# Performance work log

Hardware: AMD Instinct MI355X
Metric: run time of the kernel (lower is better)

The kernel has to match this reference:

```python
import jax, jax.numpy as jnp
import numpy as np

EPS = 1e-6
BETA = 0.25
COMMIT_W = 1.0


def setup_inputs() -> dict:
    key = jax.random.key(0)
    k1, k2, k3 = jax.random.split(key, 3)
    b, c, h, w = 8, 256, 32, 32
    n_e, e_dim = 16384, 256
    z = jax.random.normal(k1, (b, c, h, w), jnp.float32)
    # frozen_codebook = randn(n_e, e_dim) * e_dim**-0.5
    codebook = jax.random.normal(k2, (n_e, e_dim), jnp.float32) * (e_dim ** -0.5)
    # nn.Linear(e_dim, in_channels, bias=False) weight: (in_channels, e_dim)
    W = jax.random.normal(k3, (c, e_dim), jnp.float32) * (e_dim ** -0.5)
    return {"z": z, "codebook": codebook, "W": W}


def _rotate_to(src, tgt):
    # Rotation trick (Fifty et al.): rotate src onto tgt direction with a
    # detached Householder-style transform; gradient flows through src only.
    # src, tgt: (n, d)
    norm_src = jnp.linalg.norm(src, axis=-1, keepdims=True)
    norm_tgt = jnp.linalg.norm(tgt, axis=-1, keepdims=True)
    u = src / (norm_src + EPS)
    q = tgt / (norm_tgt + EPS)
    uq = u + q
    w_ = jax.lax.stop_gradient(uq / (jnp.linalg.norm(uq, axis=-1, keepdims=True) + EPS))
    u_d = jax.lax.stop_gradient(u)
    q_d = jax.lax.stop_gradient(q)
    rot = (src
           - 2.0 * jnp.sum(src * w_, axis=-1, keepdims=True) * w_
           + 2.0 * jnp.sum(src * u_d, axis=-1, keepdims=True) * q_d)
    return rot * jax.lax.stop_gradient(norm_tgt / (norm_src + EPS))


def reference(z, codebook, W):
    b, c, h, w = z.shape
    # b c h w -> (b*h*w, c)
    z_flat = jnp.transpose(z, (0, 2, 3, 1)).reshape(-1, c)
    # implicit codebook: frozen codes through linear projection
    emb = codebook @ W.T  # (n_e, c)
    # squared L2 distances (no grad needed for argmin)
    d = (jnp.sum(z_flat ** 2, axis=1, keepdims=True)
         + jnp.sum(emb ** 2, axis=1)
         - 2.0 * (z_flat @ emb.T))  # (n_tok, n_e)
    indices = jnp.argmin(d, axis=1)  # (n_tok,)
    z_q_flat = emb[indices]  # gather quantized vectors
    loss = COMMIT_W * (jnp.mean((jax.lax.stop_gradient(z_flat) - z_q_flat) ** 2)
                       + BETA * jnp.mean((z_flat - jax.lax.stop_gradient(z_q_flat)) ** 2))
    z_q_flat = _rotate_to(z_flat, z_q_flat)
    z_q = jnp.transpose(z_q_flat.reshape(b, h, w, c), (0, 3, 1, 2))
    return z_q, loss, indices
```

## Files before the change

### kernel.cpp

```cpp
#include <hip/hip_runtime.h>
#include <math.h>

#define EPSV 1e-6f
#define NTOK 8192
#define NE   16384
#define DIM  256

using short8 = __attribute__((ext_vector_type(8))) short;
using f32x4v = __attribute__((ext_vector_type(4))) float;

__device__ __forceinline__ unsigned short f2bf(float v) {
    unsigned int u = __float_as_uint(v);
    u += 0x7fffu + ((u >> 16) & 1u);
    return (unsigned short)(u >> 16);
}
__device__ __forceinline__ float bf2f(unsigned short h) {
    return __uint_as_float(((unsigned int)h) << 16);
}

__device__ __forceinline__ void gload_lds16(const void* g, void* s) {
    __builtin_amdgcn_global_load_lds(
        (const __attribute__((address_space(1))) void*)g,
        (__attribute__((address_space(3))) void*)s, 16, 0, 0);
}

__global__ __launch_bounds__(256) void k0a_transpose(
    const float* __restrict__ zin, float* __restrict__ z_flat,
    unsigned short* __restrict__ zh, unsigned short* __restrict__ zl) {
    __shared__ float tile[64][65];
    const int tid = threadIdx.x;
    const int yx0 = blockIdx.x * 64, c0 = blockIdx.y * 64, b = blockIdx.z;
    const int sub = tid >> 6, ln = tid & 63;
#pragma unroll
    for (int j = 0; j < 16; ++j) {
        int cl = j * 4 + sub;
        tile[cl][ln] = zin[((size_t)(b * 256 + c0 + cl) << 10) + yx0 + ln];
    }
    __syncthreads();
#pragma unroll
    for (int j = 0; j < 16; ++j) {
        int tl = j * 4 + sub;
        float v = tile[ln][tl];
        size_t o = (size_t)(b * 1024 + yx0 + tl) * 256 + c0 + ln;
        z_flat[o] = v;
        unsigned short h = f2bf(v);
        zh[o] = h;
        zl[o] = f2bf(v - bf2f(h));
    }
}

__global__ __launch_bounds__(256) void k0b_sz(const float* __restrict__ z_flat,
                                              float* __restrict__ sz) {
    const int w = threadIdx.x >> 6, lane = threadIdx.x & 63;
    const int t = blockIdx.x * 4 + w;
    const float4 v = *(const float4*)(z_flat + (size_t)t * 256 + lane * 4);
    double s = (double)v.x * v.x + (double)v.y * v.y + (double)v.z * v.z +
               (double)v.w * v.w;
#pragma unroll
    for (int m = 1; m < 64; m <<= 1) s += __shfl_xor(s, m);
    if (lane == 0) sz[t] = (float)s;
}

__global__ __launch_bounds__(256) void k0c_emb(
    const float* __restrict__ cb, const float* __restrict__ Wm,
    float* __restrict__ emb, unsigned short* __restrict__ eh,
    unsigned short* __restrict__ el) {
    __shared__ float cbS[64][68];
    __shared__ float wS[64][68];
    const int tid = threadIdx.x;
    const int n0 = blockIdx.x * 64, c0 = blockIdx.y * 64;
    const int tx = tid & 15, ty = tid >> 4;
    float acc[4][4] = {};
    for (int kc = 0; kc < 4; ++kc) {
        __syncthreads();
#pragma unroll
        for (int it = 0; it < 16; ++it) {
            int idx = it * 256 + tid;
            int rw = idx >> 6, kk = idx & 63;
            cbS[rw][kk] = cb[(size_t)(n0 + rw) * 256 + kc * 64 + kk];
            wS[rw][kk]  = Wm[(size_t)(c0 + rw) * 256 + kc * 64 + kk];
        }
        __syncthreads();
#pragma unroll
        for (int k4 = 0; k4 < 16; ++k4) {
            float4 ra[4], rb[4];
#pragma unroll
            for (int a = 0; a < 4; ++a)
                ra[a] = *(const float4*)&cbS[ty * 4 + a][k4 * 4];
#pragma unroll
            for (int bb = 0; bb < 4; ++bb)
                rb[bb] = *(const float4*)&wS[tx * 4 + bb][k4 * 4];
#pragma unroll
            for (int a = 0; a < 4; ++a)
#pragma unroll
                for (int bb = 0; bb < 4; ++bb)
                    acc[a][bb] += ra[a].x * rb[bb].x + ra[a].y * rb[bb].y +
                                  ra[a].z * rb[bb].z + ra[a].w * rb[bb].w;
        }
    }
#pragma unroll
    for (int a = 0; a < 4; ++a) {
        int n = n0 + ty * 4 + a;
#pragma unroll
        for (int bb = 0; bb < 4; ++bb) {
            int c = c0 + tx * 4 + bb;
            size_t o = (size_t)n * 256 + c;
            float v = acc[a][bb];
            emb[o] = v;
            unsigned short h = f2bf(v);
            eh[o] = h;
            el[o] = f2bf(v - bf2f(h));
        }
    }
}

__global__ __launch_bounds__(256) void k0d_se(const float* __restrict__ emb,
                                              float* __restrict__ se) {
    const int w = threadIdx.x >> 6, lane = threadIdx.x & 63;
    const int n = blockIdx.x * 4 + w;
    const float4 v = *(const float4*)(emb + (size_t)n * 256 + lane * 4);
    double s = (double)v.x * v.x + (double)v.y * v.y + (double)v.z * v.z +
               (double)v.w * v.w;
#pragma unroll
    for (int m = 1; m < 64; m <<= 1) s += __shfl_xor(s, m);
    if (lane == 0) se[n] = (float)s;
}

__global__ __launch_bounds__(256, 2) void k1_dist_argmin(
    const unsigned short* __restrict__ zh, const unsigned short* __restrict__ zl,
    const unsigned short* __restrict__ eh, const unsigned short* __restrict__ el,
    const float* __restrict__ sz, const float* __restrict__ se,
    float* __restrict__ pval, int* __restrict__ pidx) {
    __shared__ short8 smem[2][2048];
    const int tid = threadIdx.x;
    const int w = tid >> 6, lane = tid & 63;
    const int quad = lane >> 4, lr = lane & 15;
    const int tokBase = blockIdx.x * 128;
    const int rowBase = tokBase + w * 32;
    const int slab = blockIdx.y;
    const int slabBase = slab * 2048;

    short8 Ah[2][8], Al[2][8];
#pragma unroll
    for (int mt = 0; mt < 2; ++mt)
#pragma unroll
        for (int ks = 0; ks < 8; ++ks) {
            size_t o = (size_t)(rowBase + mt * 16 + lr) * 256 + ks * 32 + quad * 8;
            Ah[mt][ks] = *(const short8*)(zh + o);
            Al[mt][ks] = *(const short8*)(zl + o);
        }

    float szr[2][4];
#pragma unroll
    for (int mt = 0; mt < 2; ++mt)
#pragma unroll
        for (int rr = 0; rr < 4; ++rr)
            szr[mt][rr] = sz[rowBase + mt * 16 + quad * 4 + rr];

    float minv[2][4];
    int mini[2][4];
#pragma unroll
    for (int mt = 0; mt < 2; ++mt)
#pragma unroll
        for (int rr = 0; rr < 4; ++rr) {
            minv[mt][rr] = INFINITY;
            mini[mt][rr] = 0;
        }

    auto stage = [&](int buf, int ch) {
        const int colBase = slabBase + ch * 32;
#pragma unroll
        for (int i = 0; i < 8; ++i) {
            int u = i * 256 + tid;
            int fmt = u >> 10;
            int u1 = u & 1023;
            int col = u1 >> 5, kgs = u1 & 31;
            int kg = kgs ^ col;
            const unsigned short* g =
                (fmt ? el : eh) + (size_t)(colBase + col) * 256 + kg * 8;
            gload_lds16(g, (char*)&smem[buf][0] + (((size_t)i * 256 + w * 64) << 4));
        }
    };

    stage(0, 0);
    __syncthreads();

    for (int ch = 0; ch < 64; ++ch) {
        const int cur = ch & 1;
        if (ch + 1 < 64) stage(cur ^ 1, ch + 1);

        f32x4v acc[2][2];
#pragma unroll
        for (int mt = 0; mt < 2; ++mt)
#pragma unroll
            for (int nt = 0; nt < 2; ++nt)
                acc[mt][nt] = (f32x4v){0.f, 0.f, 0.f, 0.f};

#pragma unroll
        for (int ks = 0; ks < 8; ++ks) {
            short8 Bh[2], Bl[2];
#pragma unroll
            for (int nt = 0; nt < 2; ++nt) {
                int col = nt * 16 + lr;
                int kgs = (ks * 4 + quad) ^ col;
                Bh[nt] = smem[cur][col * 32 + kgs];
                Bl[nt] = smem[cur][1024 + col * 32 + kgs];
            }
#pragma unroll
            for (int mt = 0; mt < 2; ++mt)
#pragma unroll
                for (int nt = 0; nt < 2; ++nt) {
                    f32x4v a = acc[mt][nt];
                    a = __builtin_amdgcn_mfma_f32_16x16x32_bf16(Ah[mt][ks], Bh[nt], a, 0, 0, 0);
                    a = __builtin_amdgcn_mfma_f32_16x16x32_bf16(Ah[mt][ks], Bl[nt], a, 0, 0, 0);
                    a = __builtin_amdgcn_mfma_f32_16x16x32_bf16(Al[mt][ks], Bh[nt], a, 0, 0, 0);
                    acc[mt][nt] = a;
                }
        }

        const int colBase = slabBase + ch * 32;
#pragma unroll
        for (int nt = 0; nt < 2; ++nt) {
            const int colg = colBase + nt * 16 + lr;
            const float sec = se[colg];
#pragma unroll
            for (int mt = 0; mt < 2; ++mt)
#pragma unroll
                for (int rr = 0; rr < 4; ++rr) {
                    float d = __fsub_rn(__fadd_rn(szr[mt][rr], sec),
                                        2.0f * acc[mt][nt][rr]);
                    if (d < minv[mt][rr]) {
                        minv[mt][rr] = d;
                        mini[mt][rr] = colg;
                    }
                }
        }
        __syncthreads();
    }

#pragma unroll
    for (int st = 1; st < 16; st <<= 1) {
#pragma unroll
        for (int mt = 0; mt < 2; ++mt)
#pragma unroll
            for (int rr = 0; rr < 4; ++rr) {
                float ov = __shfl_xor(minv[mt][rr], st);
                int oi = __shfl_xor(mini[mt][rr], st);
                if (ov < minv[mt][rr] ||
                    (ov == minv[mt][rr] && oi < mini[mt][rr])) {
                    minv[mt][rr] = ov;
                    mini[mt][rr] = oi;
                }
            }
    }
    if (lr == 0) {
#pragma unroll
        for (int mt = 0; mt < 2; ++mt)
#pragma unroll
            for (int rr = 0; rr < 4; ++rr) {
                int row = rowBase + mt * 16 + quad * 4 + rr;
                pval[(size_t)row * 8 + slab] = minv[mt][rr];
                pidx[(size_t)row * 8 + slab] = mini[mt][rr];
            }
    }
}

__global__ __launch_bounds__(256) void k3a_token(
    const float* __restrict__ z_flat, const float* __restrict__ emb,
    const float* __restrict__ pval, const int* __restrict__ pidx,
    float* __restrict__ alpha, float* __restrict__ beta,
    int* __restrict__ idxf, float* __restrict__ out,
    float* __restrict__ lpart) {
    __shared__ float red[4];
    const int w = threadIdx.x >> 6, lane = threadIdx.x & 63;
    const int t = blockIdx.x * 4 + w;
    int best = 0;
    if (lane == 0) {
        float bv = INFINITY;
        int bi = 0;
#pragma unroll
        for (int s = 0; s < 8; ++s) {
            float v = pval[(size_t)t * 8 + s];
            int ii = pidx[(size_t)t * 8 + s];
            if (v < bv || (v == bv && ii < bi)) { bv = v; bi = ii; }
        }
        best = bi;
    }
    best = __shfl(best, 0);

    const float4 zv = *(const float4*)(z_flat + (size_t)t * 256 + lane * 4);
    const float4 ev = *(const float4*)(emb + (size_t)best * 256 + lane * 4);
    float szs = zv.x * zv.x + zv.y * zv.y + zv.z * zv.z + zv.w * zv.w;
    float ses = ev.x * ev.x + ev.y * ev.y + ev.z * ev.z + ev.w * ev.w;
    float zes = zv.x * ev.x + zv.y * ev.y + zv.z * ev.z + zv.w * ev.w;
    float dx = zv.x - ev.x, dy = zv.y - ev.y, dz = zv.z - ev.z, dw = zv.w - ev.w;
    float sqs = dx * dx + dy * dy + dz * dz + dw * dw;
#pragma unroll
    for (int m = 1; m < 64; m <<= 1) {
        szs += __shfl_xor(szs, m);
        ses += __shfl_xor(ses, m);
        zes += __shfl_xor(zes, m);
        sqs += __shfl_xor(sqs, m);
    }
    if (lane == 0) {
        float ns = sqrtf(szs), nt = sqrtf(ses);
        float inv_s = 1.0f / (ns + EPSV);
        float inv_t = 1.0f / (nt + EPSV);
        float s2 = szs * inv_s;
        float su = szs * inv_s * inv_s;
        float sq = ses * inv_t * inv_t;
        float uq = zes * inv_s * inv_t;
        float nw = sqrtf(su + sq + 2.0f * uq);
        float inv_w = 1.0f / (nw + EPSV);
        float s1 = (s2 + zes * inv_t) * inv_w;
        float scale = nt * inv_s;
        float a = scale * (1.0f - 2.0f * s1 * inv_w * inv_s);
        float bb = scale * inv_t * 2.0f * (s2 - s1 * inv_w);
        alpha[t] = a;
        beta[t] = bb;
        idxf[t] = best;
        out[2097153 + t] = (float)best;
        red[w] = sqs;
    }
    __syncthreads();
    if (threadIdx.x == 0)
        lpart[blockIdx.x] = red[0] + red[1] + red[2] + red[3];
}

__global__ __launch_bounds__(256) void k4_loss(float* __restrict__ out,
                                               const float* __restrict__ lpart) {
    __shared__ float red[4];
    const int tid = threadIdx.x;
    float s = 0.0f;
    for (int i = tid; i < 2048; i += 256) s += lpart[i];
#pragma unroll
    for (int m = 1; m < 64; m <<= 1) s += __shfl_xor(s, m);
    if ((tid & 63) == 0) red[tid >> 6] = s;
    __syncthreads();
    if (tid == 0)
        out[2097152] = 1.25f * (red[0] + red[1] + red[2] + red[3]) *
                       (1.0f / 2097152.0f);
}

__global__ __launch_bounds__(256) void k3b_zq(
    const float* __restrict__ zin, const float* __restrict__ emb,
    const float* __restrict__ alpha, const float* __restrict__ beta,
    const int* __restrict__ idxf, float* __restrict__ out) {
    const int i = blockIdx.x * 256 + threadIdx.x;
    const int c = (i >> 10) & 255;
    const int t = ((i >> 18) << 10) | (i & 1023);
    out[i] = alpha[t] * zin[i] + beta[t] * emb[(size_t)idxf[t] * 256 + c];
}

extern "C" void kernel_launch(void* const* d_in, const int* in_sizes, int n_in,
                              void* d_out, int out_size, void* d_ws,
                              size_t ws_size, hipStream_t stream) {
    (void)in_sizes; (void)n_in; (void)out_size; (void)ws_size;
    const float* zin = (const float*)d_in[0];
    const float* cb  = (const float*)d_in[1];
    const float* Wm  = (const float*)d_in[2];
    float* out = (float*)d_out;
    char* ws = (char*)d_ws;

    float*          z_flat = (float*)(ws + 0);
    unsigned short* zh     = (unsigned short*)(ws + 8388608);
    unsigned short* zl     = (unsigned short*)(ws + 12582912);
    float*          emb    = (float*)(ws + 16777216);
    unsigned short* eh     = (unsigned short*)(ws + 33554432);
    unsigned short* el     = (unsigned short*)(ws + 41943040);
    float*          sz     = (float*)(ws + 50331648);
    float*          se     = (float*)(ws + 50364416);
    float*          pval   = (float*)(ws + 50429952);
    int*            pidx   = (int*)(ws + 50692096);
    float*          alpha  = (float*)(ws + 50954240);
    float*          beta   = (float*)(ws + 50987008);
    int*            idxf   = (int*)(ws + 51019776);
    float*          lpart  = (float*)(ws + 51052544);

    k0a_transpose<<<dim3(16, 4, 8), 256, 0, stream>>>(zin, z_flat, zh, zl);
    k0b_sz<<<2048, 256, 0, stream>>>(z_flat, sz);
    k0c_emb<<<dim3(256, 4), 256, 0, stream>>>(cb, Wm, emb, eh, el);
    k0d_se<<<4096, 256, 0, stream>>>(emb, se);
    k1_dist_argmin<<<dim3(64, 8), 256, 0, stream>>>(zh, zl, eh, el, sz, se,
                                                    pval, pidx);
    k3a_token<<<2048, 256, 0, stream>>>(z_flat, emb, pval, pidx, alpha, beta,
                                        idxf, out, lpart);
    k4_loss<<<1, 256, 0, stream>>>(out, lpart);
    k3b_zq<<<8192, 256, 0, stream>>>(zin, emb, alpha, beta, idxf, out);
}
```

Baseline: 340.2 us.

## Use split-bf16 MFMA for codebook projection and drop LDS staging in distance kernel

Rewrites the emb = codebook @ W^T kernel from scalar FP32 FMAs to bf16 hi/lo split MFMA with 128x128 tiles, using a new pre-kernel that splits W into bf16 halves. The distance/argmin kernel stops staging codebook tiles through LDS with double buffering and barriers, and instead loads B fragments straight from global memory per wave. The per-token argmin merge across slabs becomes a shuffle reduction over 8 lanes. The aim is to cut FP32 ALU cost in the projection and barrier/LDS overhead in the main kernel. The risks are more global/L2 traffic from redundant per-wave loads, and small precision differences in emb from the 4-term bf16 split.

Measured after the change: 588.0 us. 1.73x slower.

```diff
diff --git a/kernel.cpp b/kernel.cpp
--- a/kernel.cpp
+++ b/kernel.cpp
@@ -22,6 +22,17 @@
     __builtin_amdgcn_global_load_lds(
         (const __attribute__((address_space(1))) void*)g,
         (__attribute__((address_space(3))) void*)s, 16, 0, 0);
+}
+
+__device__ __forceinline__ void split8(const float4 a, const float4 b,
+                                       short8& h, short8& l) {
+    float f[8] = {a.x, a.y, a.z, a.w, b.x, b.y, b.z, b.w};
+#pragma unroll
+    for (int j = 0; j < 8; ++j) {
+        unsigned short hh = f2bf(f[j]);
+        h[j] = (short)hh;
+        l[j] = (short)f2bf(f[j] - bf2f(hh));
+    }
 }
 
 __global__ __launch_bounds__(256) void k0a_transpose(
@@ -61,57 +72,107 @@
     if (lane == 0) sz[t] = (float)s;
 }
 
-__global__ __launch_bounds__(256) void k0c_emb(
-    const float* __restrict__ cb, const float* __restrict__ Wm,
-    float* __restrict__ emb, unsigned short* __restrict__ eh,
-    unsigned short* __restrict__ el) {
-    __shared__ float cbS[64][68];
-    __shared__ float wS[64][68];
+__global__ __launch_bounds__(256) void k0pre(const float* __restrict__ Wm,
+                                             unsigned short* __restrict__ wh,
+                                             unsigned short* __restrict__ wl) {
+    const int i = (blockIdx.x * 256 + threadIdx.x) * 4;
+    const float4 v = *(const float4*)(Wm + i);
+    float f[4] = {v.x, v.y, v.z, v.w};
+#pragma unroll
+    for (int j = 0; j < 4; ++j) {
+        unsigned short h = f2bf(f[j]);
+        wh[i + j] = h;
+        wl[i + j] = f2bf(f[j] - bf2f(h));
+    }
+}
+
+__global__ __launch_bounds__(256, 2) void k0c_emb(
+    const float* __restrict__ cb, const unsigned short* __restrict__ wh,
+    const unsigned short* __restrict__ wl, float* __restrict__ emb,
+    unsigned short* __restrict__ eh, unsigned short* __restrict__ el) {
+    __shared__ char smemC[65536];
     const int tid = threadIdx.x;
-    const int n0 = blockIdx.x * 64, c0 = blockIdx.y * 64;
-    const int tx = tid & 15, ty = tid >> 4;
-    float acc[4][4] = {};
+    const int w = tid >> 6, lane = tid & 63;
+    const int quad = lane >> 4, lr = lane & 15;
+    const int wr = w & 1, wc = w >> 1;
+    const int n0 = blockIdx.x * 128, c0 = blockIdx.y * 128;
+
+    f32x4v acc[4][4];
+#pragma unroll
+    for (int mt = 0; mt < 4; ++mt)
+#pragma unroll
+        for (int nt = 0; nt < 4; ++nt)
+            acc[mt][nt] = (f32x4v){0.f, 0.f, 0.f, 0.f};
+
     for (int kc = 0; kc < 4; ++kc) {
         __syncthreads();
 #pragma unroll
-        for (int it = 0; it < 16; ++it) {
-            int idx = it * 256 + tid;
-            int rw = idx >> 6, kk = idx & 63;
-            cbS[rw][kk] = cb[(size_t)(n0 + rw) * 256 + kc * 64 + kk];
-            wS[rw][kk]  = Wm[(size_t)(c0 + rw) * 256 + kc * 64 + kk];
+        for (int i = 0; i < 16; ++i) {
+            int s = i * 4 + w;
+            int u = s * 64 + lane;
+            const void* g;
+            if (s < 32) {
+                int kg = u >> 7, row = u & 127;
+                g = cb + (size_t)(n0 + row) * 256 + kc * 64 + kg * 4;
+            } else if (s < 48) {
+                int u1 = u - 2048;
+                int kg = u1 >> 7, row = u1 & 127;
+                g = wh + (size_t)(c0 + row) * 256 + kc * 64 + kg * 8;
+            } else {
+                int u2 = u - 3072;
+                int kg = u2 >> 7, row = u2 & 127;
+                g = wl + (size_t)(c0 + row) * 256 + kc * 64 + kg * 8;
+            }
+            gload_lds16(g, smemC + ((size_t)u << 4));
         }
         __syncthreads();
 #pragma unroll
-        for (int k4 = 0; k4 < 16; ++k4) {
-            float4 ra[4], rb[4];
-#pragma unroll
-            for (int a = 0; a < 4; ++a)
-                ra[a] = *(const float4*)&cbS[ty * 4 + a][k4 * 4];
-#pragma unroll
-            for (int bb = 0; bb < 4; ++bb)
-                rb[bb] = *(const float4*)&wS[tx * 4 + bb][k4 * 4];
-#pragma unroll
-            for (int a = 0; a < 4; ++a)
-#pragma unroll
-                for (int bb = 0; bb < 4; ++bb)
-                    acc[a][bb] += ra[a].x * rb[bb].x + ra[a].y * rb[bb].y +
-                                  ra[a].z * rb[bb].z + ra[a].w * rb[bb].w;
-        }
-    }
-#pragma unroll
-    for (int a = 0; a < 4; ++a) {
-        int n = n0 + ty * 4 + a;
-#pragma unroll
-        for (int bb = 0; bb < 4; ++bb) {
-            int c = c0 + tx * 4 + bb;
-            size_t o = (size_t)n * 256 + c;
-            float v = acc[a][bb];
-            emb[o] = v;
-            unsigned short h = f2bf(v);
-            eh[o] = h;
-            el[o] = f2bf(v - bf2f(h));
-        }
-    }
+        for (int ks = 0; ks < 2; ++ks) {
+            short8 Ah[4], Al[4], Bh[4], Bl[4];
+#pragma unroll
+            for (int mt = 0; mt < 4; ++mt) {
+                int m = wr * 64 + mt * 16 + lr;
+                int kg2 = ks * 8 + quad * 2;
+                float4 f0 = *(const float4*)(smemC + (((size_t)kg2 * 128 + m) << 4));
+                float4 f1 = *(const float4*)(smemC + ((((size_t)kg2 + 1) * 128 + m) << 4));
+                split8(f0, f1, Ah[mt], Al[mt]);
+            }
+#pragma unroll
+            for (int nt = 0; nt < 4; ++nt) {
+                int n = wc * 64 + nt * 16 + lr;
+                int ku = (ks * 4 + quad) * 128 + n;
+                Bh[nt] = *(const short8*)(smemC + (((size_t)2048 + ku) << 4));
+                Bl[nt] = *(const short8*)(smemC + (((size_t)3072 + ku) << 4));
+            }
+#pragma unroll
+            for (int mt = 0; mt < 4; ++mt)
+#pragma unroll
+                for (int nt = 0; nt < 4; ++nt) {
+                    f32x4v a = acc[mt][nt];
+                    a = __builtin_amdgcn_mfma_f32_16x16x32_bf16(Ah[mt], Bh[nt], a, 0, 0, 0);
+                    a = __builtin_amdgcn_mfma_f32_16x16x32_bf16(Ah[mt], Bl[nt], a, 0, 0, 0);
+                    a = __builtin_amdgcn_mfma_f32_16x16x32_bf16(Al[mt], Bh[nt], a, 0, 0, 0);
+                    a = __builtin_amdgcn_mfma_f32_16x16x32_bf16(Al[mt], Bl[nt], a, 0, 0, 0);
+                    acc[mt][nt] = a;
+                }
+        }
+    }
+#pragma unroll
+    for (int mt = 0; mt < 4; ++mt)
+#pragma unroll
+        for (int rr = 0; rr < 4; ++rr) {
+            int row = n0 + wr * 64 + mt * 16 + quad * 4 + rr;
+#pragma unroll
+            for (int nt = 0; nt < 4; ++nt) {
+                int col = c0 + wc * 64 + nt * 16 + lr;
+                size_t o = (size_t)row * 256 + col;
+                float v = acc[mt][nt][rr];
+                emb[o] = v;
+                unsigned short h = f2bf(v);
+                eh[o] = h;
+                el[o] = f2bf(v - bf2f(h));
+            }
+        }
 }
 
 __global__ __launch_bounds__(256) void k0d_se(const float* __restrict__ emb,
@@ -131,7 +192,6 @@
     const unsigned short* __restrict__ eh, const unsigned short* __restrict__ el,
     const float* __restrict__ sz, const float* __restrict__ se,
     float* __restrict__ pval, int* __restrict__ pidx) {
-    __shared__ short8 smem[2][2048];
     const int tid = threadIdx.x;
     const int w = tid >> 6, lane = tid & 63;
     const int quad = lane >> 4, lr = lane & 15;
@@ -167,28 +227,13 @@
             mini[mt][rr] = 0;
         }
 
-    auto stage = [&](int buf, int ch) {
-        const int colBase = slabBase + ch * 32;
-#pragma unroll
-        for (int i = 0; i < 8; ++i) {
-            int u = i * 256 + tid;
-            int fmt = u >> 10;
-            int u1 = u & 1023;
-            int col = u1 >> 5, kgs = u1 & 31;
-            int kg = kgs ^ col;
-            const unsigned short* g =
-                (fmt ? el : eh) + (size_t)(colBase + col) * 256 + kg * 8;
-            gload_lds16(g, (char*)&smem[buf][0] + (((size_t)i * 256 + w * 64) << 4));
-        }
-    };
-
-    stage(0, 0);
-    __syncthreads();
+    const char* pH = (const char*)eh + (((size_t)(slabBase + lr)) << 9) + (quad << 4);
+    const char* pL = (const char*)el + (((size_t)(slabBase + lr)) << 9) + (quad << 4);
+    const float* pSe = se + slabBase + lr;
 
     for (int ch = 0; ch < 64; ++ch) {
-        const int cur = ch & 1;
-        if (ch + 1 < 64) stage(cur ^ 1, ch + 1);
-
+        const float se0 = pSe[0];
+        const float se1 = pSe[16];
         f32x4v acc[2][2];
 #pragma unroll
         for (int mt = 0; mt < 2; ++mt)
@@ -198,31 +243,29 @@
 
 #pragma unroll
         for (int ks = 0; ks < 8; ++ks) {
-            short8 Bh[2], Bl[2];
-#pragma unroll
-            for (int nt = 0; nt < 2; ++nt) {
-                int col = nt * 16 + lr;
-                int kgs = (ks * 4 + quad) ^ col;
-                Bh[nt] = smem[cur][col * 32 + kgs];
-                Bl[nt] = smem[cur][1024 + col * 32 + kgs];
-            }
-#pragma unroll
-            for (int mt = 0; mt < 2; ++mt)
-#pragma unroll
-                for (int nt = 0; nt < 2; ++nt) {
-                    f32x4v a = acc[mt][nt];
-                    a = __builtin_amdgcn_mfma_f32_16x16x32_bf16(Ah[mt][ks], Bh[nt], a, 0, 0, 0);
-                    a = __builtin_amdgcn_mfma_f32_16x16x32_bf16(Ah[mt][ks], Bl[nt], a, 0, 0, 0);
-                    a = __builtin_amdgcn_mfma_f32_16x16x32_bf16(Al[mt][ks], Bh[nt], a, 0, 0, 0);
-                    acc[mt][nt] = a;
-                }
+            short8 bh0 = *(const short8*)(pH + ks * 64);
+            short8 bh1 = *(const short8*)(pH + 8192 + ks * 64);
+            short8 bl0 = *(const short8*)(pL + ks * 64);
+            short8 bl1 = *(const short8*)(pL + 8192 + ks * 64);
+#pragma unroll
+            for (int mt = 0; mt < 2; ++mt) {
+                f32x4v a0 = acc[mt][0], a1 = acc[mt][1];
+                a0 = __builtin_amdgcn_mfma_f32_16x16x32_bf16(Ah[mt][ks], bh0, a0, 0, 0, 0);
+                a0 = __builtin_amdgcn_mfma_f32_16x16x32_bf16(Ah[mt][ks], bl0, a0, 0, 0, 0);
+                a0 = __builtin_amdgcn_mfma_f32_16x16x32_bf16(Al[mt][ks], bh0, a0, 0, 0, 0);
+                a1 = __builtin_amdgcn_mfma_f32_16x16x32_bf16(Ah[mt][ks], bh1, a1, 0, 0, 0);
+                a1 = __builtin_amdgcn_mfma_f32_16x16x32_bf16(Ah[mt][ks], bl1, a1, 0, 0, 0);
+                a1 = __builtin_amdgcn_mfma_f32_16x16x32_bf16(Al[mt][ks], bh1, a1, 0, 0, 0);
+                acc[mt][0] = a0;
+                acc[mt][1] = a1;
+            }
         }
 
         const int colBase = slabBase + ch * 32;
 #pragma unroll
         for (int nt = 0; nt < 2; ++nt) {
             const int colg = colBase + nt * 16 + lr;
-            const float sec = se[colg];
+            const float sec = nt ? se1 : se0;
 #pragma unroll
             for (int mt = 0; mt < 2; ++mt)
 #pragma unroll
@@ -235,7 +278,9 @@
                     }
                 }
         }
-        __syncthreads();
+        pH += 16384;
+        pL += 16384;
+        pSe += 32;
     }
 
 #pragma unroll
@@ -274,19 +319,20 @@
     __shared__ float red[4];
     const int w = threadIdx.x >> 6, lane = threadIdx.x & 63;
     const int t = blockIdx.x * 4 + w;
-    int best = 0;
-    if (lane == 0) {
-        float bv = INFINITY;
-        int bi = 0;
-#pragma unroll
-        for (int s = 0; s < 8; ++s) {
-            float v = pval[(size_t)t * 8 + s];
-            int ii = pidx[(size_t)t * 8 + s];
-            if (v < bv || (v == bv && ii < bi)) { bv = v; bi = ii; }
-        }
-        best = bi;
-    }
-    best = __shfl(best, 0);
+
+    float bv = INFINITY;
+    int bi = 0x7fffffff;
+    if (lane < 8) {
+        bv = pval[(size_t)t * 8 + lane];
+        bi = pidx[(size_t)t * 8 + lane];
+    }
+#pragma unroll
+    for (int st = 1; st < 8; st <<= 1) {
+        float ov = __shfl_xor(bv, st);
+        int oi = __shfl_xor(bi, st);
+        if (ov < bv || (ov == bv && oi < bi)) { bv = ov; bi = oi; }
+    }
+    const int best = __shfl(bi, 0);
 
     const float4 zv = *(const float4*)(z_flat + (size_t)t * 256 + lane * 4);
     const float4 ev = *(const float4*)(emb + (size_t)best * 256 + lane * 4);
@@ -376,10 +422,13 @@
     float*          beta   = (float*)(ws + 50987008);
     int*            idxf   = (int*)(ws + 51019776);
     float*          lpart  = (float*)(ws + 51052544);
+    unsigned short* wh     = (unsigned short*)(ws + 51060736);
+    unsigned short* wl     = (unsigned short*)(ws + 51191808);
 
     k0a_transpose<<<dim3(16, 4, 8), 256, 0, stream>>>(zin, z_flat, zh, zl);
     k0b_sz<<<2048, 256, 0, stream>>>(z_flat, sz);
-    k0c_emb<<<dim3(256, 4), 256, 0, stream>>>(cb, Wm, emb, eh, el);
+    k0pre<<<64, 256, 0, stream>>>(Wm, wh, wl);
+    k0c_emb<<<dim3(128, 2), 256, 0, stream>>>(cb, wh, wl, emb, eh, el);
     k0d_se<<<4096, 256, 0, stream>>>(emb, se);
     k1_dist_argmin<<<dim3(64, 8), 256, 0, stream>>>(zh, zl, eh, el, sz, se,
                                                     pval, pidx);
```
